# Kernel optimization log

Measured on AMD Instinct MI355X. Metric: run time of the kernel, lower is better.

Reference implementation:

```python
import jax, jax.numpy as jnp
import numpy as np
import math

B, H, W, C = 8, 32, 32, 512
NUM_HEAD_CHANNELS = 64
NUM_HEADS = C // NUM_HEAD_CHANNELS  # 8
HEAD_DIM = C // NUM_HEADS            # 64
NUM_GROUPS = max(1, C // 16)         # 32
EPS = 1e-6  # flax GroupNorm default epsilon


def setup_inputs() -> dict:
    key = jax.random.key(0)
    ks = jax.random.split(key, 7)
    s = lambda fan: 1.0 / math.sqrt(fan)
    return {
        "x": jax.random.normal(ks[0], (B, H, W, C), jnp.float32),
        "gn_scale": jnp.ones((C,), jnp.float32),
        "gn_bias": jnp.zeros((C,), jnp.float32),
        "w_qkv": jax.random.normal(ks[1], (C, 3 * C), jnp.float32) * s(C),
        "b_qkv": jnp.zeros((3 * C,), jnp.float32),
        "w_out": jax.random.normal(ks[2], (C, C), jnp.float32) * s(C),
        "b_out": jnp.zeros((C,), jnp.float32),
    }


def _group_norm(x, scale, bias):
    # x: (B,H,W,C); normalize per (batch, group) over spatial + in-group channels
    b, h, w, c = x.shape
    xg = x.reshape(b, h * w, NUM_GROUPS, c // NUM_GROUPS)
    mu = jnp.mean(xg, axis=(1, 3), keepdims=True)
    var = jnp.var(xg, axis=(1, 3), keepdims=True)
    xn = (xg - mu) * jax.lax.rsqrt(var + EPS)
    return xn.reshape(b, h, w, c) * scale + bias


def reference(x, gn_scale, gn_bias, w_qkv, b_qkv, w_out, b_out):
    b, h, w, c = x.shape
    seq = h * w
    x_flat = x.reshape(b, seq, c)
    x_norm = _group_norm(x, gn_scale, gn_bias).reshape(b, seq, c)
    qkv = x_norm @ w_qkv + b_qkv                      # (b, seq, 3c)
    q, k, v = jnp.split(qkv, 3, axis=-1)
    scale = 1.0 / math.sqrt(HEAD_DIM)

    def to_heads(t):
        return t.reshape(b, seq, NUM_HEADS, HEAD_DIM).transpose(0, 2, 1, 3)

    q, k, v = to_heads(q), to_heads(k), to_heads(v)
    # NOTE: scale applied to both q and k, matching the original module
    weight = jnp.einsum('bhld,bhsd->bhls', q * scale, k * scale)
    weight = jax.nn.softmax(weight, axis=-1)
    out = jnp.einsum('bhls,bhsd->bhld', weight, v)
    out = out.transpose(0, 2, 1, 3).reshape(b, seq, c)
    out = out @ w_out + b_out
    return (x_flat + out).reshape(b, h, w, c)
```

## Files before the change

kernel.cpp:

```cpp
#include <hip/hip_runtime.h>
#include <hip/hip_bf16.h>

#define SEQ   1024
#define CH    512
#define NHEAD 8
#define HDIM  64
#define BATCH 8

using short8  = __attribute__((ext_vector_type(8))) short;
using short4v = __attribute__((ext_vector_type(4))) short;
using floatx4 = __attribute__((ext_vector_type(4))) float;

__device__ inline unsigned short f2bf(float f) {
  __hip_bfloat16 h = __float2bfloat16(f);
  return __builtin_bit_cast(unsigned short, h);
}

__device__ inline void load_lds16(const void* g, void* l) {
  __builtin_amdgcn_global_load_lds(
      (const __attribute__((address_space(1))) unsigned int*)g,
      (__attribute__((address_space(3))) unsigned int*)l, 16, 0, 0);
}

__global__ __launch_bounds__(256) void prep_stats_kernel(
    const float* __restrict__ wqkv, const float* __restrict__ wout,
    const float* __restrict__ x,
    unsigned short* __restrict__ wqkvt, unsigned short* __restrict__ woutt,
    float2* __restrict__ stats) {
  __shared__ float SH[32 * 33 + 8];
  const int blk = blockIdx.x, tid = threadIdx.x;

  if (blk >= 2048) {
    const float* src; unsigned short* dst; int C, bx, by;
    if (blk < 2816) { int t = blk - 2048; src = wqkv; dst = wqkvt; C = 1536; bx = t % 48; by = t / 48; }
    else { int t = blk - 2816; src = wout; dst = woutt; C = 512; bx = t & 15; by = t >> 4; }
    float (*T)[33] = (float(*)[33])SH;
    int tx = tid & 31, ty = tid >> 5;
    for (int j = 0; j < 4; ++j)
      T[ty + j * 8][tx] = src[(size_t)(by * 32 + ty + j * 8) * C + bx * 32 + tx];
    __syncthreads();
    for (int j = 0; j < 4; ++j)
      dst[(size_t)(bx * 32 + ty + j * 8) * 512 + by * 32 + tx] = f2bf(T[tx][ty + j * 8]);
    return;
  }

  const int bg = blk >> 3, chunk = blk & 7;
  const int b = bg >> 5, g = bg & 31;
  const size_t base = (size_t)b * SEQ * CH + (size_t)chunk * 128 * CH + g * 16;

  float s = 0.f, sq = 0.f;
  for (int i = 0; i < 2; ++i) {
    int c = i * 256 + tid;
    int r = c >> 2, c4 = (c & 3) * 4;
    float4 v = *(const float4*)(x + base + (size_t)r * CH + c4);
    s  += v.x + v.y + v.z + v.w;
    sq += v.x * v.x + v.y * v.y + v.z * v.z + v.w * v.w;
  }
  for (int off = 1; off < 64; off <<= 1) {
    s  += __shfl_xor(s, off);
    sq += __shfl_xor(sq, off);
  }
  float* ls = SH + 1056;
  float* lq = SH + 1060;
  int wid = tid >> 6, lane = tid & 63;
  if (lane == 0) { ls[wid] = s; lq[wid] = sq; }
  __syncthreads();
  if (tid == 0) {
    float2 p;
    p.x = ls[0] + ls[1] + ls[2] + ls[3];
    p.y = lq[0] + lq[1] + lq[2] + lq[3];
    stats[(bg << 3) + chunk] = p;
  }
}

__global__ __launch_bounds__(256) void prep_apply_kernel(
    const float* __restrict__ x, const float* __restrict__ gsc,
    const float* __restrict__ gbs, const float2* __restrict__ stats,
    unsigned short* __restrict__ xn) {
  const int blk = blockIdx.x, tid = threadIdx.x;
  const int bg = blk >> 3, chunk = blk & 7;
  const int b = bg >> 5, g = bg & 31;

  float ts = 0.f, tq = 0.f;
  for (int i = 0; i < 8; ++i) {
    float2 p = stats[(bg << 3) + i];
    ts += p.x; tq += p.y;
  }
  const float inv_n = 1.0f / 16384.0f;
  float mean = ts * inv_n;
  float var  = tq * inv_n - mean * mean;
  float rstd = rsqrtf(var + 1e-6f);

  const size_t base = (size_t)b * SEQ * CH + (size_t)chunk * 128 * CH + g * 16;
  const size_t obase = (size_t)(b * SEQ + chunk * 128) * CH + g * 16;
  int c4 = (tid & 3) * 4;
  float4 sc = *(const float4*)(gsc + g * 16 + c4);
  float4 bs = *(const float4*)(gbs + g * 16 + c4);
  for (int i = 0; i < 2; ++i) {
    int c = i * 256 + tid;
    int r = c >> 2;
    float4 v = *(const float4*)(x + base + (size_t)r * CH + c4);
    ushort4 o;
    o.x = f2bf((v.x - mean) * rstd * sc.x + bs.x);
    o.y = f2bf((v.y - mean) * rstd * sc.y + bs.y);
    o.z = f2bf((v.z - mean) * rstd * sc.z + bs.z);
    o.w = f2bf((v.w - mean) * rstd * sc.w + bs.w);
    *(ushort4*)(xn + obase + (size_t)r * CH + c4) = o;
  }
}

template <int EPI, int MTILE>
__global__ __launch_bounds__(256) void gemm_bt_kernel(
    const unsigned short* __restrict__ A, const unsigned short* __restrict__ Bt,
    int K, int N,
    const float* __restrict__ bias, const float* __restrict__ resid,
    float* __restrict__ outf,
    unsigned short* __restrict__ qb, unsigned short* __restrict__ kb,
    unsigned short* __restrict__ vtb) {
  constexpr int SMSZ = (MTILE == 128) ? 17408 : 16896;
  constexpr int NI   = (MTILE == 128) ? 4 : 2;
  __shared__ alignas(16) unsigned short SM[SMSZ];
  unsigned short* LA = SM;
  unsigned short* LB = SM + MTILE * 64;

  const int tid = threadIdx.x;
  const int wid = tid >> 6, lane = tid & 63;
  const int quad = lane >> 4, m16 = lane & 15;
  const int sw = m16 & 7;
  const int wm = (MTILE == 128) ? (wid & 1) * 64 : 0;
  const int wn = (MTILE == 128) ? (wid >> 1) * 64 : wid * 32;
  const int m0 = blockIdx.x * MTILE, n0 = blockIdx.y * 128;

  floatx4 acc[4][NI];
  for (int i = 0; i < 4; ++i)
    for (int j = 0; j < NI; ++j) acc[i][j] = 0.f;

  for (int k0 = 0; k0 < K; k0 += 64) {
    for (int i = 0; i < MTILE / 32; ++i) {
      int c = i * 256 + tid;
      int r = c >> 3, kc = c & 7;
      load_lds16(A + (size_t)(m0 + r) * K + k0 + ((kc ^ (r & 7)) << 3), &LA[c << 3]);
    }
    for (int i = 0; i < 4; ++i) {
      int c = i * 256 + tid;
      int r = c >> 3, kc = c & 7;
      load_lds16(Bt + (size_t)(n0 + r) * K + k0 + ((kc ^ (r & 7)) << 3), &LB[c << 3]);
    }
    __syncthreads();
    for (int kq = 0; kq < 2; ++kq) {
      int csw = (((kq << 2) + quad) ^ sw) << 3;
      short8 af[4], bf[NI];
      for (int mi = 0; mi < 4; ++mi)
        af[mi] = *(const short8*)&LA[(wm + mi * 16 + m16) * 64 + csw];
      for (int ni = 0; ni < NI; ++ni)
        bf[ni] = *(const short8*)&LB[(wn + ni * 16 + m16) * 64 + csw];
      for (int mi = 0; mi < 4; ++mi)
        for (int ni = 0; ni < NI; ++ni)
          acc[mi][ni] = __builtin_amdgcn_mfma_f32_16x16x32_bf16(af[mi], bf[ni], acc[mi][ni], 0, 0, 0);
    }
    __syncthreads();
  }

  const int b = m0 >> 10;
  if (EPI == 0) {
    const int part = n0 >> 9;
    if (part < 2) {
      const float qscale = (part == 0) ? 0.0225421381f : 1.0f;
      unsigned short* dst = (part == 0) ? qb : kb;
      for (int mi = 0; mi < 4; ++mi)
        for (int ni = 0; ni < 4; ++ni) {
          int ln = wn + ni * 16 + m16;
          float bb = bias[n0 + ln];
          for (int reg = 0; reg < 4; ++reg)
            SM[(wm + mi * 16 + quad * 4 + reg) * 136 + ln] =
                f2bf((acc[mi][ni][reg] + bb) * qscale);
        }
      __syncthreads();
      const int colb = n0 & 511;
      for (int j = 0; j < 8; ++j) {
        int c = j * 256 + tid;
        int m = c >> 4, n8 = (c & 15) * 8;
        int h = (colb + n8) >> 6, d = n8 & 63;
        int sp = (m0 & 1023) + m;
        int4 v = *(const int4*)&SM[m * 136 + n8];
        *(int4*)(dst + (((size_t)(b * NHEAD + h)) * SEQ + sp) * HDIM + d) = v;
      }
    } else {
      for (int mi = 0; mi < 4; ++mi)
        for (int ni = 0; ni < 4; ++ni) {
          int ln = wn + ni * 16 + m16;
          float bb = bias[n0 + ln];
          int mblk = (wm >> 4) + mi;
          int sbase = 32 * (mblk >> 1) + 8 * quad + 4 * (mblk & 1);
          for (int reg = 0; reg < 4; ++reg)
            SM[ln * 136 + sbase + reg] = f2bf(acc[mi][ni][reg] + bb);
        }
      __syncthreads();
      int hbase = (n0 - 1024) >> 6;
      for (int j = 0; j < 8; ++j) {
        int c = j * 256 + tid;
        int ld = c >> 4, sp8 = (c & 15) * 8;
        int h = hbase + (ld >> 6), d = ld & 63;
        int4 v = *(const int4*)&SM[ld * 136 + sp8];
        *(int4*)(vtb + ((size_t)(b * NHEAD + h) * HDIM + d) * SEQ + (m0 & 1023) + sp8) = v;
      }
    }
  } else {
    float* SMf = (float*)SM;
    for (int mi = 0; mi < 4; ++mi)
      for (int ni = 0; ni < NI; ++ni) {
        int ln = wn + ni * 16 + m16;
        float bb = bias[n0 + ln];
        for (int reg = 0; reg < 4; ++reg)
          SMf[(mi * 16 + quad * 4 + reg) * 132 + ln] = acc[mi][ni][reg] + bb;
      }
    __syncthreads();
    for (int j = 0; j < 8; ++j) {
      int c = j * 256 + tid;
      int m = c >> 5, n4 = (c & 31) * 4;
      size_t idx = (size_t)(m0 + m) * N + n0 + n4;
      float4 v = *(const float4*)&SMf[m * 132 + n4];
      float4 rr = *(const float4*)&resid[idx];
      v.x += rr.x; v.y += rr.y; v.z += rr.z; v.w += rr.w;
      *(float4*)&outf[idx] = v;
    }
  }
}

__global__ __launch_bounds__(512) void attn_kernel(
    const unsigned short* __restrict__ qb, const unsigned short* __restrict__ kb,
    const unsigned short* __restrict__ vtb, unsigned short* __restrict__ ao) {
  const int head = blockIdx.x, qt = blockIdx.y;
  const int b = head >> 3, h = head & 7;
  const int tid = threadIdx.x;
  const int wid = tid >> 6, lane = tid & 63;
  const int quad = lane >> 4, m16 = lane & 15;
  const int sw = m16 & 7;

  __shared__ alignas(16) unsigned short sK[8192];
  __shared__ alignas(16) unsigned short sV[8192];

  const unsigned short* kbase = kb  + (size_t)head * SEQ * HDIM;
  const unsigned short* vbase = vtb + (size_t)head * HDIM * SEQ;

  const size_t qrow = (size_t)head * SEQ + qt * 128 + wid * 16 + m16;
  short8 aq0 = *(const short8*)(qb + qrow * HDIM + quad * 8);
  short8 aq1 = *(const short8*)(qb + qrow * HDIM + 32 + quad * 8);

  float lacc = 0.f;
  floatx4 o[4];
  for (int df = 0; df < 4; ++df) o[df] = 0.f;

  for (int kt = 0; kt < 8; ++kt) {
    for (int i = 0; i < 2; ++i) {
      int c = i * 512 + tid;
      int r = c >> 3, kc = c & 7;
      load_lds16(kbase + (kt * 128 + r) * HDIM + ((kc ^ (r & 7)) << 3), &sK[c << 3]);
    }
    for (int i = 0; i < 2; ++i) {
      int c = i * 512 + tid;
      int d = c >> 4, kc = c & 15;
      load_lds16(vbase + d * SEQ + kt * 128 + ((kc ^ (d & 7)) << 3), &sV[c << 3]);
    }
    __syncthreads();

    short8 pf32[4];
    for (int sf = 0; sf < 8; ++sf) {
      const int rb = (sf * 16 + m16) * 64;
      short8 k0 = *(const short8*)&sK[rb + ((quad ^ sw) << 3)];
      short8 k1 = *(const short8*)&sK[rb + (((4 + quad) ^ sw) << 3)];
      floatx4 s = 0.f;
      s = __builtin_amdgcn_mfma_f32_16x16x32_bf16(k0, aq0, s, 0, 0, 0);
      s = __builtin_amdgcn_mfma_f32_16x16x32_bf16(k1, aq1, s, 0, 0, 0);
      const int u = sf >> 1, t4 = (sf & 1) * 4;
      for (int r = 0; r < 4; ++r) {
        float p = exp2f(s[r]);
        lacc += p;
        pf32[u][t4 + r] = (short)f2bf(p);
      }
    }

    for (int u = 0; u < 4; ++u) {
      const int chunk = ((u * 4 + quad) ^ sw) << 3;
      for (int df = 0; df < 4; ++df) {
        short8 bv = *(const short8*)&sV[(df * 16 + m16) * 128 + chunk];
        o[df] = __builtin_amdgcn_mfma_f32_16x16x32_bf16(pf32[u], bv, o[df], 0, 0, 0);
      }
    }
    __syncthreads();
  }

  lacc += __shfl_xor(lacc, 16);
  lacc += __shfl_xor(lacc, 32);
  lacc = 1.0f / lacc;
  float l0 = __shfl(lacc, quad * 4 + 0);
  float l1 = __shfl(lacc, quad * 4 + 1);
  float l2 = __shfl(lacc, quad * 4 + 2);
  float l3 = __shfl(lacc, quad * 4 + 3);
  int qg = qt * 128 + wid * 16 + quad * 4;
  for (int df = 0; df < 4; ++df) {
    int col = h * HDIM + df * 16 + m16;
    size_t base = (size_t)(b * SEQ + qg) * CH + col;
    ao[base + 0 * CH] = f2bf(o[df][0] * l0);
    ao[base + 1 * CH] = f2bf(o[df][1] * l1);
    ao[base + 2 * CH] = f2bf(o[df][2] * l2);
    ao[base + 3 * CH] = f2bf(o[df][3] * l3);
  }
}

extern "C" void kernel_launch(void* const* d_in, const int* in_sizes, int n_in,
                              void* d_out, int out_size, void* d_ws, size_t ws_size,
                              hipStream_t stream) {
  const float* x    = (const float*)d_in[0];
  const float* gsc  = (const float*)d_in[1];
  const float* gbs  = (const float*)d_in[2];
  const float* wqkv = (const float*)d_in[3];
  const float* bqkv = (const float*)d_in[4];
  const float* wout = (const float*)d_in[5];
  const float* bout = (const float*)d_in[6];
  float* out = (float*)d_out;

  char* ws = (char*)d_ws;
  unsigned short* xn    = (unsigned short*)(ws);
  unsigned short* wqkvt = (unsigned short*)(ws + 8388608);
  unsigned short* woutt = (unsigned short*)(ws + 9961472);
  unsigned short* qb    = (unsigned short*)(ws + 10485760);
  unsigned short* kb    = (unsigned short*)(ws + 18874368);
  unsigned short* vtb   = (unsigned short*)(ws + 27262976);
  unsigned short* ao    = (unsigned short*)(ws + 35651584);
  float2*         stats = (float2*)(ws + 44040192);

  prep_stats_kernel<<<3072, 256, 0, stream>>>(wqkv, wout, x, wqkvt, woutt, stats);
  prep_apply_kernel<<<2048, 256, 0, stream>>>(x, gsc, gbs, stats, xn);
  gemm_bt_kernel<0, 128><<<dim3(64, 12), 256, 0, stream>>>(
      xn, wqkvt, 512, 1536, bqkv, nullptr, nullptr, qb, kb, vtb);
  attn_kernel<<<dim3(64, 8), 512, 0, stream>>>(qb, kb, vtb, ao);
  gemm_bt_kernel<1, 64><<<dim3(128, 4), 256, 0, stream>>>(
      ao, woutt, 512, 512, bout, x, out, nullptr, nullptr, nullptr);
}
```

Baseline: 149.8 us.

## Fuse GroupNorm stats and apply into one kernel, double-buffer attention K/V tiles

Merges the two GroupNorm prep kernels into a single 1024-thread kernel. Each block holds a whole (batch, group) slice in LDS, so x is read from global memory once and the stats round-trip and one launch go away. The weight transpose moves to 64x64 tiles. The attention kernel double-buffers K/V in LDS so the next tile's loads overlap compute, and it raises wave priority around the MFMAs. The risks are lower occupancy from the 64KB LDS in prep and from doubled LDS in attention, and only 512 blocks in prep.

```diff
diff --git a/kernel.cpp b/kernel.cpp
--- a/kernel.cpp
+++ b/kernel.cpp
@@ -22,37 +22,38 @@
       (__attribute__((address_space(3))) unsigned int*)l, 16, 0, 0);
 }
 
-__global__ __launch_bounds__(256) void prep_stats_kernel(
+__global__ __launch_bounds__(1024) void prep_kernel(
     const float* __restrict__ wqkv, const float* __restrict__ wout,
-    const float* __restrict__ x,
+    const float* __restrict__ x, const float* __restrict__ gsc,
+    const float* __restrict__ gbs,
     unsigned short* __restrict__ wqkvt, unsigned short* __restrict__ woutt,
-    float2* __restrict__ stats) {
-  __shared__ float SH[32 * 33 + 8];
+    unsigned short* __restrict__ xn) {
+  __shared__ float SH[16416];
   const int blk = blockIdx.x, tid = threadIdx.x;
 
-  if (blk >= 2048) {
+  if (blk >= 256) {
     const float* src; unsigned short* dst; int C, bx, by;
-    if (blk < 2816) { int t = blk - 2048; src = wqkv; dst = wqkvt; C = 1536; bx = t % 48; by = t / 48; }
-    else { int t = blk - 2816; src = wout; dst = woutt; C = 512; bx = t & 15; by = t >> 4; }
-    float (*T)[33] = (float(*)[33])SH;
-    int tx = tid & 31, ty = tid >> 5;
+    if (blk < 448) { int t = blk - 256; src = wqkv; dst = wqkvt; C = 1536; bx = t % 24; by = t / 24; }
+    else           { int t = blk - 448; src = wout; dst = woutt; C = 512;  bx = t & 7;  by = t >> 3; }
+    float (*T)[65] = (float(*)[65])SH;
+    int tx = tid & 63, ty = tid >> 6;
     for (int j = 0; j < 4; ++j)
-      T[ty + j * 8][tx] = src[(size_t)(by * 32 + ty + j * 8) * C + bx * 32 + tx];
+      T[ty + j * 16][tx] = src[(size_t)(by * 64 + ty + j * 16) * C + bx * 64 + tx];
     __syncthreads();
     for (int j = 0; j < 4; ++j)
-      dst[(size_t)(bx * 32 + ty + j * 8) * 512 + by * 32 + tx] = f2bf(T[tx][ty + j * 8]);
+      dst[(size_t)(bx * 64 + ty + j * 16) * 512 + by * 64 + tx] = f2bf(T[tx][ty + j * 16]);
     return;
   }
 
-  const int bg = blk >> 3, chunk = blk & 7;
-  const int b = bg >> 5, g = bg & 31;
-  const size_t base = (size_t)b * SEQ * CH + (size_t)chunk * 128 * CH + g * 16;
+  const int b = blk >> 5, g = blk & 31;
+  const size_t base = (size_t)b * SEQ * CH + g * 16;
 
   float s = 0.f, sq = 0.f;
-  for (int i = 0; i < 2; ++i) {
-    int c = i * 256 + tid;
-    int r = c >> 2, c4 = (c & 3) * 4;
+  for (int i = 0; i < 4; ++i) {
+    int c = (i << 10) + tid;
+    int r = c >> 2, c4 = (c & 3) << 2;
     float4 v = *(const float4*)(x + base + (size_t)r * CH + c4);
+    *(float4*)&SH[c << 2] = v;
     s  += v.x + v.y + v.z + v.w;
     sq += v.x * v.x + v.y * v.y + v.z * v.z + v.w * v.w;
   }
@@ -60,52 +61,29 @@
     s  += __shfl_xor(s, off);
     sq += __shfl_xor(sq, off);
   }
-  float* ls = SH + 1056;
-  float* lq = SH + 1060;
-  int wid = tid >> 6, lane = tid & 63;
-  if (lane == 0) { ls[wid] = s; lq[wid] = sq; }
+  const int wid = tid >> 6, lane = tid & 63;
+  if (lane == 0) { SH[16384 + wid] = s; SH[16400 + wid] = sq; }
   __syncthreads();
-  if (tid == 0) {
-    float2 p;
-    p.x = ls[0] + ls[1] + ls[2] + ls[3];
-    p.y = lq[0] + lq[1] + lq[2] + lq[3];
-    stats[(bg << 3) + chunk] = p;
-  }
-}
-
-__global__ __launch_bounds__(256) void prep_apply_kernel(
-    const float* __restrict__ x, const float* __restrict__ gsc,
-    const float* __restrict__ gbs, const float2* __restrict__ stats,
-    unsigned short* __restrict__ xn) {
-  const int blk = blockIdx.x, tid = threadIdx.x;
-  const int bg = blk >> 3, chunk = blk & 7;
-  const int b = bg >> 5, g = bg & 31;
-
   float ts = 0.f, tq = 0.f;
-  for (int i = 0; i < 8; ++i) {
-    float2 p = stats[(bg << 3) + i];
-    ts += p.x; tq += p.y;
-  }
+  for (int i = 0; i < 16; ++i) { ts += SH[16384 + i]; tq += SH[16400 + i]; }
   const float inv_n = 1.0f / 16384.0f;
   float mean = ts * inv_n;
   float var  = tq * inv_n - mean * mean;
   float rstd = rsqrtf(var + 1e-6f);
 
-  const size_t base = (size_t)b * SEQ * CH + (size_t)chunk * 128 * CH + g * 16;
-  const size_t obase = (size_t)(b * SEQ + chunk * 128) * CH + g * 16;
-  int c4 = (tid & 3) * 4;
+  int c4 = (tid & 3) << 2;
   float4 sc = *(const float4*)(gsc + g * 16 + c4);
   float4 bs = *(const float4*)(gbs + g * 16 + c4);
-  for (int i = 0; i < 2; ++i) {
-    int c = i * 256 + tid;
+  for (int i = 0; i < 4; ++i) {
+    int c = (i << 10) + tid;
     int r = c >> 2;
-    float4 v = *(const float4*)(x + base + (size_t)r * CH + c4);
+    float4 v = *(const float4*)&SH[c << 2];
     ushort4 o;
     o.x = f2bf((v.x - mean) * rstd * sc.x + bs.x);
     o.y = f2bf((v.y - mean) * rstd * sc.y + bs.y);
     o.z = f2bf((v.z - mean) * rstd * sc.z + bs.z);
     o.w = f2bf((v.w - mean) * rstd * sc.w + bs.w);
-    *(ushort4*)(xn + obase + (size_t)r * CH + c4) = o;
+    *(ushort4*)(xn + base + (size_t)r * CH + c4) = o;
   }
 }
 
@@ -237,8 +215,8 @@
   const int quad = lane >> 4, m16 = lane & 15;
   const int sw = m16 & 7;
 
-  __shared__ alignas(16) unsigned short sK[8192];
-  __shared__ alignas(16) unsigned short sV[8192];
+  __shared__ alignas(16) unsigned short sK[2][8192];
+  __shared__ alignas(16) unsigned short sV[2][8192];
 
   const unsigned short* kbase = kb  + (size_t)head * SEQ * HDIM;
   const unsigned short* vbase = vtb + (size_t)head * HDIM * SEQ;
@@ -251,27 +229,44 @@
   floatx4 o[4];
   for (int df = 0; df < 4; ++df) o[df] = 0.f;
 
+  for (int i = 0; i < 2; ++i) {
+    int c = i * 512 + tid;
+    int r = c >> 3, kc = c & 7;
+    load_lds16(kbase + r * HDIM + ((kc ^ (r & 7)) << 3), &sK[0][c << 3]);
+  }
+  for (int i = 0; i < 2; ++i) {
+    int c = i * 512 + tid;
+    int d = c >> 4, kc = c & 15;
+    load_lds16(vbase + d * SEQ + ((kc ^ (d & 7)) << 3), &sV[0][c << 3]);
+  }
+  __syncthreads();
+
+  int buf = 0;
   for (int kt = 0; kt < 8; ++kt) {
-    for (int i = 0; i < 2; ++i) {
-      int c = i * 512 + tid;
-      int r = c >> 3, kc = c & 7;
-      load_lds16(kbase + (kt * 128 + r) * HDIM + ((kc ^ (r & 7)) << 3), &sK[c << 3]);
-    }
-    for (int i = 0; i < 2; ++i) {
-      int c = i * 512 + tid;
-      int d = c >> 4, kc = c & 15;
-      load_lds16(vbase + d * SEQ + kt * 128 + ((kc ^ (d & 7)) << 3), &sV[c << 3]);
-    }
-    __syncthreads();
+    if (kt < 7) {
+      const int nb = buf ^ 1, kn = kt + 1;
+      for (int i = 0; i < 2; ++i) {
+        int c = i * 512 + tid;
+        int r = c >> 3, kc = c & 7;
+        load_lds16(kbase + (kn * 128 + r) * HDIM + ((kc ^ (r & 7)) << 3), &sK[nb][c << 3]);
+      }
+      for (int i = 0; i < 2; ++i) {
+        int c = i * 512 + tid;
+        int d = c >> 4, kc = c & 15;
+        load_lds16(vbase + d * SEQ + kn * 128 + ((kc ^ (d & 7)) << 3), &sV[nb][c << 3]);
+      }
+    }
 
     short8 pf32[4];
     for (int sf = 0; sf < 8; ++sf) {
       const int rb = (sf * 16 + m16) * 64;
-      short8 k0 = *(const short8*)&sK[rb + ((quad ^ sw) << 3)];
-      short8 k1 = *(const short8*)&sK[rb + (((4 + quad) ^ sw) << 3)];
+      short8 k0 = *(const short8*)&sK[buf][rb + ((quad ^ sw) << 3)];
+      short8 k1 = *(const short8*)&sK[buf][rb + (((4 + quad) ^ sw) << 3)];
       floatx4 s = 0.f;
+      __builtin_amdgcn_s_setprio(1);
       s = __builtin_amdgcn_mfma_f32_16x16x32_bf16(k0, aq0, s, 0, 0, 0);
       s = __builtin_amdgcn_mfma_f32_16x16x32_bf16(k1, aq1, s, 0, 0, 0);
+      __builtin_amdgcn_s_setprio(0);
       const int u = sf >> 1, t4 = (sf & 1) * 4;
       for (int r = 0; r < 4; ++r) {
         float p = exp2f(s[r]);
@@ -282,12 +277,15 @@
 
     for (int u = 0; u < 4; ++u) {
       const int chunk = ((u * 4 + quad) ^ sw) << 3;
+      __builtin_amdgcn_s_setprio(1);
       for (int df = 0; df < 4; ++df) {
-        short8 bv = *(const short8*)&sV[(df * 16 + m16) * 128 + chunk];
+        short8 bv = *(const short8*)&sV[buf][(df * 16 + m16) * 128 + chunk];
         o[df] = __builtin_amdgcn_mfma_f32_16x16x32_bf16(pf32[u], bv, o[df], 0, 0, 0);
       }
-    }
-    __syncthreads();
+      __builtin_amdgcn_s_setprio(0);
+    }
+    __syncthreads();
+    buf ^= 1;
   }
 
   lacc += __shfl_xor(lacc, 16);
@@ -328,10 +326,8 @@
   unsigned short* kb    = (unsigned short*)(ws + 18874368);
   unsigned short* vtb   = (unsigned short*)(ws + 27262976);
   unsigned short* ao    = (unsigned short*)(ws + 35651584);
-  float2*         stats = (float2*)(ws + 44040192);
-
-  prep_stats_kernel<<<3072, 256, 0, stream>>>(wqkv, wout, x, wqkvt, woutt, stats);
-  prep_apply_kernel<<<2048, 256, 0, stream>>>(x, gsc, gbs, stats, xn);
+
+  prep_kernel<<<512, 1024, 0, stream>>>(wqkv, wout, x, gsc, gbs, wqkvt, woutt, xn);
   gemm_bt_kernel<0, 128><<<dim3(64, 12), 256, 0, stream>>>(
       xn, wqkvt, 512, 1536, bqkv, nullptr, nullptr, qb, kb, vtb);
   attn_kernel<<<dim3(64, 8), 512, 0, stream>>>(qb, kb, vtb, ao);
```

Result: no change. 149.6 us (-0.1%).
